# Performance work log

Measured on AMD Instinct MI355X. Metric: run time of the kernel, lower is better.

The kernel has to match this reference:

```python
import jax, jax.numpy as jnp
import numpy as np

N = 2048      # nodes: 8 sequences x 256 tokens
E = 524288    # edges: dense attention graph, 8 * 256^2
H = 8         # heads
DK = 64       # per-head dim


def setup_inputs() -> dict:
    key = jax.random.key(0)
    k1, k2, k3, k4, k5 = jax.random.split(key, 5)
    q = jax.random.normal(k1, (N, H, DK), dtype=jnp.float32)
    k = jax.random.normal(k2, (N, H, DK), dtype=jnp.float32)
    v = jax.random.normal(k3, (N, H, DK), dtype=jnp.float32)
    edge_src = jax.random.randint(k4, (E,), 0, N, dtype=jnp.int32)
    edge_dst = jax.random.randint(k5, (E,), 0, N, dtype=jnp.int32)
    return {"q": q, "k": k, "v": v, "edge_src": edge_src, "edge_dst": edge_dst}


def reference(q, k, v, edge_src, edge_dst):
    # src_dot_dst('k','q','score'): per-edge dot product over head dim -> [E, H]
    score = jnp.einsum('ehd,ehd->eh', k[edge_src], q[edge_dst])
    # scaled_exp('score', sqrt(d_k)): exp(clamp(score / sqrt(d_k), -10, 10))
    score = jnp.exp(jnp.clip(score / jnp.sqrt(jnp.float32(DK)), -10.0, 10.0))
    # send_and_recv: wv = sum_dst(v_src * score), z = sum_dst(score)
    wv = jax.ops.segment_sum(v[edge_src] * score[:, :, None], edge_dst, num_segments=N)  # [N, H, DK]
    z = jax.ops.segment_sum(score, edge_dst, num_segments=N)  # [N, H]
    # post_func normalization: attention output per node
    return wv / z[:, :, None]
```

## Files before the change

kernel.cpp:

```cpp
#include <hip/hip_runtime.h>

#define NNODES 2048
#define NHEAD 8
#define DKDIM 64

typedef unsigned int uint;
typedef unsigned short ushort;
typedef unsigned char uchar;
typedef __fp16 h2 __attribute__((ext_vector_type(2)));
typedef __fp16 h8 __attribute__((ext_vector_type(8)));
typedef float f16v __attribute__((ext_vector_type(16)));

#define KSCALE 0.18033688011112042f
#define CLAMP2 14.426950408889634f

__device__ __forceinline__ uint pk2(float a, float b) {
    union { h2 h; uint u; } x; x.h = __builtin_amdgcn_cvt_pkrtz(a, b); return x.u;
}

__global__ void prep1(const float* __restrict__ k, uint4* __restrict__ kc,
                      uint4* __restrict__ A4) {
    int i = blockIdx.x * 256 + threadIdx.x;
    int dim8 = i & 7, node = (i >> 3) & 2047, h = i >> 14;
    const float* src = k + (size_t)node * 512 + h * 64 + dim8 * 8;
    float4 f0 = *(const float4*)src;
    float4 f1 = *(const float4*)(src + 4);
    uint4 o;
    o.x = pk2(f0.x * KSCALE, f0.y * KSCALE);
    o.y = pk2(f0.z * KSCALE, f0.w * KSCALE);
    o.z = pk2(f1.x * KSCALE, f1.y * KSCALE);
    o.w = pk2(f1.z * KSCALE, f1.w * KSCALE);
    kc[(h * 2048 + node) * 8 + dim8] = o;
    uint4 zz = {0u, 0u, 0u, 0u};
    A4[i] = zz;
}

__global__ void prep2(const float* __restrict__ v, ushort* __restrict__ vt,
                      const int* __restrict__ es, const int* __restrict__ ed,
                      uint* __restrict__ A32, int E) {
    __shared__ float tile[64][65];
    int b = blockIdx.x;
    int t = threadIdx.x;
    if (b < 256) {
        int h = b & 7, tn = b >> 3;
        int nl = t >> 2, dq = (t & 3) * 16;
        const float* src = v + ((size_t)(tn * 64 + nl)) * 512 + h * 64 + dq;
#pragma unroll
        for (int i = 0; i < 4; ++i) {
            float4 f = *(const float4*)(src + i * 4);
            tile[nl][dq + i * 4 + 0] = f.x;
            tile[nl][dq + i * 4 + 1] = f.y;
            tile[nl][dq + i * 4 + 2] = f.z;
            tile[nl][dq + i * 4 + 3] = f.w;
        }
        __syncthreads();
        int dim = t >> 2, nq = (t & 3) * 16;
        uint wv[8];
#pragma unroll
        for (int i = 0; i < 8; ++i)
            wv[i] = pk2(tile[nq + 2 * i][dim], tile[nq + 2 * i + 1][dim]);
        char* base = (char*)vt + ((size_t)(b & 7) * 64 + dim) * 4096 + (b >> 3) * 128;
        int nb0 = (t & 3) * 2;
        uint4 lo = { wv[0], wv[1], wv[2], wv[3] };
        uint4 hi = { wv[4], wv[5], wv[6], wv[7] };
        *(uint4*)(base + nb0 * 16) = lo;
        *(uint4*)(base + nb0 * 16 + 16) = hi;
    } else {
        int i = (b - 256) * 256 + t;
        if (i < E) {
            uint idx = (uint)ed[i] * 2048u + (uint)es[i];
            atomicAdd(&A32[idx >> 3], 1u << ((idx & 7) * 4));
        }
    }
}

__global__ void __launch_bounds__(512, 4) attn_kernel(
    const float* __restrict__ q, const ushort* __restrict__ kc, const ushort* __restrict__ vt,
    const uchar* __restrict__ A8, float* __restrict__ out) {
    __shared__ __align__(16) char LK[2][2][8192];
    __shared__ __align__(16) char LV[2][2][8192];

    int b = blockIdx.x;
    int j = b & 7, idx = b >> 3;
    int dt = (j & 3) * 8 + (idx >> 2);
    int h = (j >> 2) * 4 + (idx & 3);
    int dst0 = dt * 64;
    int t = threadIdx.x;
    int w = t >> 6, half = w >> 2;
    int u = w & 3, sr = u >> 1, dc = u & 1;
    int l = t & 63, lm = l & 31, hi = l >> 5;
    int ht = t & 255;

    const char* kH = (const char*)kc + (size_t)h * 262144;
    const char* vH = (const char*)vt + (size_t)h * 262144;
    const char* aRow = (const char*)A8 + (size_t)(dst0 + dc * 32 + lm) * 1024 + sr * 16;

    h8 qf[4];
    {
        const float* qp = q + (size_t)(dst0 + dc * 32 + lm) * 512 + h * 64 + hi * 8;
#pragma unroll
        for (int jq = 0; jq < 4; ++jq) {
            float4 f0 = *(const float4*)(qp + jq * 16);
            float4 f1 = *(const float4*)(qp + jq * 16 + 4);
            union { uint u4[4]; h8 v; } U;
            U.u4[0] = pk2(f0.x, f0.y); U.u4[1] = pk2(f0.z, f0.w);
            U.u4[2] = pk2(f1.x, f1.y); U.u4[3] = pk2(f1.z, f1.w);
            qf[jq] = U.v;
        }
    }

    f16v of[2];
#pragma unroll
    for (int dg = 0; dg < 2; ++dg)
#pragma unroll
        for (int i = 0; i < 16; ++i) of[dg][i] = 0.f;
    float z = 0.f;

    int r0 = ht >> 3, b0 = ht & 7;
    int ts0 = half * 16;
    uint4 kr[2], vr[2];
    uint4 ac, an;

#pragma unroll
    for (int jj = 0; jj < 2; ++jj) {
        int row = r0 + jj * 32;
        kr[jj] = *(const uint4*)(kH + (size_t)(ts0 * 64 + row) * 128 + b0 * 16);
        vr[jj] = *(const uint4*)(vH + (size_t)row * 4096 + ts0 * 128 + b0 * 16);
        *(uint4*)(LK[half][0] + row * 128 + (b0 ^ (row & 7)) * 16) = kr[jj];
        *(uint4*)(LV[half][0] + row * 128 + (b0 ^ (row & 7)) * 16) = vr[jj];
    }
    ac = *(const uint4*)(aRow + ts0 * 32);
    __syncthreads();

    for (int it = 0; it < 16; ++it) {
        int cur = it & 1;
        int ts = ts0 + it;
        if (it < 15) {
#pragma unroll
            for (int jj = 0; jj < 2; ++jj) {
                int row = r0 + jj * 32;
                kr[jj] = *(const uint4*)(kH + (size_t)((ts + 1) * 64 + row) * 128 + b0 * 16);
                vr[jj] = *(const uint4*)(vH + (size_t)row * 4096 + (ts + 1) * 128 + b0 * 16);
            }
            an = *(const uint4*)(aRow + (ts + 1) * 32);
        }

        f16v sacc;
#pragma unroll
        for (int i = 0; i < 16; ++i) sacc[i] = 0.f;
        __builtin_amdgcn_s_setprio(1);
#pragma unroll
        for (int jq = 0; jq < 4; ++jq) {
            h8 kf = *(const h8*)(LK[half][cur] + (sr * 32 + lm) * 128 +
                                 (((2 * jq + hi) ^ (lm & 7)) * 16));
            sacc = __builtin_amdgcn_mfma_f32_32x32x16_f16(kf, qf[jq], sacc, 0, 0, 0);
        }
        __builtin_amdgcn_s_setprio(0);

        uint W[4][2];
        {
            const uint* aw4 = (const uint*)&ac;
#pragma unroll
            for (int G = 0; G < 4; ++G) {
                uint aw = aw4[G];
                float ee[4];
#pragma unroll
                for (int j2 = 0; j2 < 4; ++j2) {
                    float sc = fminf(fmaxf(sacc[4 * G + j2], -CLAMP2), CLAMP2);
                    ee[j2] = exp2f(sc) * (float)((aw >> (16 * hi + 4 * j2)) & 15u);
                    z += ee[j2];
                }
                W[G][0] = pk2(ee[0], ee[1]);
                W[G][1] = pk2(ee[2], ee[3]);
            }
        }
        uint Wx[4][2];
#pragma unroll
        for (int G = 0; G < 4; ++G) {
            Wx[G][0] = __shfl_xor(W[G][0], 32);
            Wx[G][1] = __shfl_xor(W[G][1], 32);
        }

        __builtin_amdgcn_s_setprio(1);
#pragma unroll
        for (int ks = 0; ks < 2; ++ks) {
            union { uint u4[4]; h8 v; } S;
            S.u4[0] = hi ? Wx[2 * ks + 1][0] : W[2 * ks][0];
            S.u4[1] = hi ? Wx[2 * ks + 1][1] : W[2 * ks][1];
            S.u4[2] = hi ? W[2 * ks + 1][0] : Wx[2 * ks][0];
            S.u4[3] = hi ? W[2 * ks + 1][1] : Wx[2 * ks][1];
#pragma unroll
            for (int dg = 0; dg < 2; ++dg) {
                h8 vf = *(const h8*)(LV[half][cur] + (dg * 32 + lm) * 128 +
                                     (((sr * 4 + ks * 2 + hi) ^ (lm & 7)) * 16));
                of[dg] = __builtin_amdgcn_mfma_f32_32x32x16_f16(vf, S.v, of[dg], 0, 0, 0);
            }
        }
        __builtin_amdgcn_s_setprio(0);

        if (it < 15) {
            int nb = cur ^ 1;
#pragma unroll
            for (int jj = 0; jj < 2; ++jj) {
                int row = r0 + jj * 32;
                *(uint4*)(LK[half][nb] + row * 128 + (b0 ^ (row & 7)) * 16) = kr[jj];
                *(uint4*)(LV[half][nb] + row * 128 + (b0 ^ (row & 7)) * 16) = vr[jj];
            }
            ac = an;
        }
        __syncthreads();
    }

    z += __shfl_xor(z, 32);

    float* CL = (float*)&LK[0][0][0];
    float* CLz = (float*)&LV[0][0][0];
    int gid = half * 2 + sr;
    for (int p = 0; p < 4; ++p) {
        if (gid == p) {
#pragma unroll
            for (int dg = 0; dg < 2; ++dg)
#pragma unroll
                for (int reg = 0; reg < 16; ++reg) {
                    int dim = dg * 32 + (reg & 3) + 8 * (reg >> 2) + 4 * hi;
                    int idx2 = (dc * 32 + lm) * 68 + dim;
                    if (p == 0) CL[idx2] = of[dg][reg];
                    else CL[idx2] += of[dg][reg];
                }
            if (hi == 0) {
                if (p == 0) CLz[dc * 32 + lm] = z;
                else CLz[dc * 32 + lm] += z;
            }
        }
        __syncthreads();
    }

    {
        int dst = t >> 3, d8 = t & 7;
        float inv = 1.0f / CLz[dst];
        float4 o0 = *(float4*)(CL + dst * 68 + d8 * 8);
        float4 o1 = *(float4*)(CL + dst * 68 + d8 * 8 + 4);
        o0.x *= inv; o0.y *= inv; o0.z *= inv; o0.w *= inv;
        o1.x *= inv; o1.y *= inv; o1.z *= inv; o1.w *= inv;
        float* op = out + (size_t)(dst0 + dst) * 512 + h * 64 + d8 * 8;
        *(float4*)op = o0;
        *(float4*)(op + 4) = o1;
    }
}


extern "C" void kernel_launch(void* const* d_in, const int* in_sizes, int n_in,
                              void* d_out, int out_size, void* d_ws, size_t ws_size,
                              hipStream_t stream) {
    const float* q = (const float*)d_in[0];
    const float* k = (const float*)d_in[1];
    const float* v = (const float*)d_in[2];
    const int* esrc = (const int*)d_in[3];
    const int* edst = (const int*)d_in[4];
    float* out = (float*)d_out;
    const int E = in_sizes[3];

    uchar* A8 = (uchar*)d_ws;
    ushort* kc = (ushort*)(A8 + (size_t)NNODES * NNODES / 2);
    ushort* vt = kc + (size_t)NHEAD * NNODES * DKDIM;

    prep1<<<512, 256, 0, stream>>>(k, (uint4*)kc, (uint4*)A8);
    prep2<<<2304, 256, 0, stream>>>(v, vt, esrc, edst, (uint*)A8, E);
    attn_kernel<<<256, 512, 0, stream>>>(q, kc, vt, A8, out);
}
```

Before: 63.64 us.

## Pre-swizzle K/V into MFMA fragment layout and load directly to registers

The prep kernels now write K and V in the exact per-lane MFMA operand order, so the attention kernel loads fragments straight from global memory into registers. This drops the LDS double-buffering and the per-iteration __syncthreads. The K and V prep and the adjacency zeroing are merged into one kernel, and the edge histogram moves to its own launch. Launch bounds are lowered to 2 blocks per SM to make room for more registers. The cost is global-load latency that is only partly hidden by prefetching K one step ahead, while V is loaded in the same iteration it is used.

Measured after the change: 55.49 us. -12.8%, faster.

```diff
diff --git a/kernel.cpp b/kernel.cpp
--- a/kernel.cpp
+++ b/kernel.cpp
@@ -18,33 +18,31 @@
     union { h2 h; uint u; } x; x.h = __builtin_amdgcn_cvt_pkrtz(a, b); return x.u;
 }
 
-__global__ void prep1(const float* __restrict__ k, uint4* __restrict__ kc,
-                      uint4* __restrict__ A4) {
-    int i = blockIdx.x * 256 + threadIdx.x;
-    int dim8 = i & 7, node = (i >> 3) & 2047, h = i >> 14;
-    const float* src = k + (size_t)node * 512 + h * 64 + dim8 * 8;
-    float4 f0 = *(const float4*)src;
-    float4 f1 = *(const float4*)(src + 4);
-    uint4 o;
-    o.x = pk2(f0.x * KSCALE, f0.y * KSCALE);
-    o.y = pk2(f0.z * KSCALE, f0.w * KSCALE);
-    o.z = pk2(f1.x * KSCALE, f1.y * KSCALE);
-    o.w = pk2(f1.z * KSCALE, f1.w * KSCALE);
-    kc[(h * 2048 + node) * 8 + dim8] = o;
-    uint4 zz = {0u, 0u, 0u, 0u};
-    A4[i] = zz;
-}
-
-__global__ void prep2(const float* __restrict__ v, ushort* __restrict__ vt,
-                      const int* __restrict__ es, const int* __restrict__ ed,
-                      uint* __restrict__ A32, int E) {
+__global__ void prep12(const float* __restrict__ k, const float* __restrict__ v,
+                       uint4* __restrict__ kc4, uint4* __restrict__ vt4,
+                       uint4* __restrict__ A4) {
     __shared__ float tile[64][65];
-    int b = blockIdx.x;
-    int t = threadIdx.x;
-    if (b < 256) {
-        int h = b & 7, tn = b >> 3;
+    int b = blockIdx.x, t = threadIdx.x;
+    if (b < 512) {
+        int i = b * 256 + t;
+        int f = i >> 6, l = i & 63;
+        int jq = f & 3, sr = (f >> 2) & 1, ts = (f >> 3) & 31, h = f >> 8;
+        int node = ts * 64 + sr * 32 + (l & 31);
+        int dim0 = (2 * jq + (l >> 5)) * 8;
+        const float* src = k + (size_t)node * 512 + h * 64 + dim0;
+        float4 f0 = *(const float4*)src;
+        float4 f1 = *(const float4*)(src + 4);
+        uint4 o;
+        o.x = pk2(f0.x * KSCALE, f0.y * KSCALE);
+        o.y = pk2(f0.z * KSCALE, f0.w * KSCALE);
+        o.z = pk2(f1.x * KSCALE, f1.y * KSCALE);
+        o.w = pk2(f1.z * KSCALE, f1.w * KSCALE);
+        kc4[(size_t)f * 64 + l] = o;
+    } else if (b < 768) {
+        int bv = b - 512;
+        int h = bv & 7, tn = bv >> 3;
         int nl = t >> 2, dq = (t & 3) * 16;
-        const float* src = v + ((size_t)(tn * 64 + nl)) * 512 + h * 64 + dq;
+        const float* src = v + (size_t)(tn * 64 + nl) * 512 + h * 64 + dq;
 #pragma unroll
         for (int i = 0; i < 4; ++i) {
             float4 f = *(const float4*)(src + i * 4);
@@ -54,31 +52,42 @@
             tile[nl][dq + i * 4 + 3] = f.w;
         }
         __syncthreads();
-        int dim = t >> 2, nq = (t & 3) * 16;
-        uint wv[8];
-#pragma unroll
-        for (int i = 0; i < 8; ++i)
-            wv[i] = pk2(tile[nq + 2 * i][dim], tile[nq + 2 * i + 1][dim]);
-        char* base = (char*)vt + ((size_t)(b & 7) * 64 + dim) * 4096 + (b >> 3) * 128;
-        int nb0 = (t & 3) * 2;
-        uint4 lo = { wv[0], wv[1], wv[2], wv[3] };
-        uint4 hi = { wv[4], wv[5], wv[6], wv[7] };
-        *(uint4*)(base + nb0 * 16) = lo;
-        *(uint4*)(base + nb0 * 16 + 16) = hi;
+#pragma unroll
+        for (int rep = 0; rep < 2; ++rep) {
+            int slot = rep * 256 + t;
+            int fsub = slot >> 6, l = slot & 63;
+            int srv = fsub >> 2, ks = (fsub >> 1) & 1, dg = fsub & 1;
+            int dim = dg * 32 + (l & 31);
+            int s8 = (srv * 4 + ks * 2 + (l >> 5)) * 8;
+            uint4 o;
+            o.x = pk2(tile[s8 + 0][dim], tile[s8 + 1][dim]);
+            o.y = pk2(tile[s8 + 2][dim], tile[s8 + 3][dim]);
+            o.z = pk2(tile[s8 + 4][dim], tile[s8 + 5][dim]);
+            o.w = pk2(tile[s8 + 6][dim], tile[s8 + 7][dim]);
+            int fV = (h * 32 + tn) * 8 + srv * 4 + ks * 2 + dg;
+            vt4[(size_t)fV * 64 + l] = o;
+        }
     } else {
-        int i = (b - 256) * 256 + t;
-        if (i < E) {
-            uint idx = (uint)ed[i] * 2048u + (uint)es[i];
-            atomicAdd(&A32[idx >> 3], 1u << ((idx & 7) * 4));
-        }
-    }
-}
-
-__global__ void __launch_bounds__(512, 4) attn_kernel(
-    const float* __restrict__ q, const ushort* __restrict__ kc, const ushort* __restrict__ vt,
+        uint4 zz = {0u, 0u, 0u, 0u};
+        A4[(size_t)(b - 768) * 512 + t] = zz;
+        A4[(size_t)(b - 768) * 512 + t + 256] = zz;
+    }
+}
+
+__global__ void histA(const int* __restrict__ es, const int* __restrict__ ed,
+                      uint* __restrict__ A32, int E) {
+    int i = blockIdx.x * 256 + threadIdx.x;
+    if (i < E) {
+        uint idx = (uint)ed[i] * 2048u + (uint)es[i];
+        atomicAdd(&A32[idx >> 3], 1u << ((idx & 7) * 4));
+    }
+}
+
+__global__ void __launch_bounds__(512, 2) attn_kernel(
+    const float* __restrict__ q, const char* __restrict__ kc, const char* __restrict__ vt,
     const uchar* __restrict__ A8, float* __restrict__ out) {
-    __shared__ __align__(16) char LK[2][2][8192];
-    __shared__ __align__(16) char LV[2][2][8192];
+    __shared__ float CL[64 * 68];
+    __shared__ float CLz[64];
 
     int b = blockIdx.x;
     int j = b & 7, idx = b >> 3;
@@ -89,11 +98,12 @@
     int w = t >> 6, half = w >> 2;
     int u = w & 3, sr = u >> 1, dc = u & 1;
     int l = t & 63, lm = l & 31, hi = l >> 5;
-    int ht = t & 255;
-
-    const char* kH = (const char*)kc + (size_t)h * 262144;
-    const char* vH = (const char*)vt + (size_t)h * 262144;
-    const char* aRow = (const char*)A8 + (size_t)(dst0 + dc * 32 + lm) * 1024 + sr * 16;
+
+    int ts0 = half * 16;
+    const char* kBase = kc + ((size_t)(h * 32 + ts0) * 8 + sr * 4) * 1024 + l * 16;
+    const char* vBase = vt + ((size_t)(h * 32 + ts0) * 8 + sr * 4) * 1024 + l * 16;
+    const char* aRow = (const char*)A8 + (size_t)(dst0 + dc * 32 + lm) * 1024 + sr * 16
+                       + ts0 * 32;
 
     h8 qf[4];
     {
@@ -116,34 +126,23 @@
         for (int i = 0; i < 16; ++i) of[dg][i] = 0.f;
     float z = 0.f;
 
-    int r0 = ht >> 3, b0 = ht & 7;
-    int ts0 = half * 16;
-    uint4 kr[2], vr[2];
+    uint4 kcur[4], knxt[4], vcur[4];
     uint4 ac, an;
 
 #pragma unroll
-    for (int jj = 0; jj < 2; ++jj) {
-        int row = r0 + jj * 32;
-        kr[jj] = *(const uint4*)(kH + (size_t)(ts0 * 64 + row) * 128 + b0 * 16);
-        vr[jj] = *(const uint4*)(vH + (size_t)row * 4096 + ts0 * 128 + b0 * 16);
-        *(uint4*)(LK[half][0] + row * 128 + (b0 ^ (row & 7)) * 16) = kr[jj];
-        *(uint4*)(LV[half][0] + row * 128 + (b0 ^ (row & 7)) * 16) = vr[jj];
-    }
-    ac = *(const uint4*)(aRow + ts0 * 32);
-    __syncthreads();
+    for (int jq = 0; jq < 4; ++jq)
+        kcur[jq] = *(const uint4*)(kBase + jq * 1024);
+    ac = *(const uint4*)aRow;
 
     for (int it = 0; it < 16; ++it) {
-        int cur = it & 1;
-        int ts = ts0 + it;
-        if (it < 15) {
-#pragma unroll
-            for (int jj = 0; jj < 2; ++jj) {
-                int row = r0 + jj * 32;
-                kr[jj] = *(const uint4*)(kH + (size_t)((ts + 1) * 64 + row) * 128 + b0 * 16);
-                vr[jj] = *(const uint4*)(vH + (size_t)row * 4096 + (ts + 1) * 128 + b0 * 16);
-            }
-            an = *(const uint4*)(aRow + (ts + 1) * 32);
-        }
+        size_t toff = (size_t)it * 8192;
+#pragma unroll
+        for (int ks = 0; ks < 2; ++ks)
+#pragma unroll
+            for (int dg = 0; dg < 2; ++dg)
+                vcur[ks * 2 + dg] = *(const uint4*)(vBase + toff + (ks * 2 + dg) * 1024);
+        int itn = (it < 15) ? it + 1 : it;
+        an = *(const uint4*)(aRow + itn * 32);
 
         f16v sacc;
 #pragma unroll
@@ -151,11 +150,14 @@
         __builtin_amdgcn_s_setprio(1);
 #pragma unroll
         for (int jq = 0; jq < 4; ++jq) {
-            h8 kf = *(const h8*)(LK[half][cur] + (sr * 32 + lm) * 128 +
-                                 (((2 * jq + hi) ^ (lm & 7)) * 16));
-            sacc = __builtin_amdgcn_mfma_f32_32x32x16_f16(kf, qf[jq], sacc, 0, 0, 0);
+            union { uint4 u; h8 v; } KF; KF.u = kcur[jq];
+            sacc = __builtin_amdgcn_mfma_f32_32x32x16_f16(KF.v, qf[jq], sacc, 0, 0, 0);
         }
         __builtin_amdgcn_s_setprio(0);
+
+#pragma unroll
+        for (int jq = 0; jq < 4; ++jq)
+            knxt[jq] = *(const uint4*)(kBase + (size_t)itn * 8192 + jq * 1024);
 
         uint W[4][2];
         {
@@ -191,30 +193,19 @@
             S.u4[3] = hi ? W[2 * ks + 1][1] : Wx[2 * ks][1];
 #pragma unroll
             for (int dg = 0; dg < 2; ++dg) {
-                h8 vf = *(const h8*)(LV[half][cur] + (dg * 32 + lm) * 128 +
-                                     (((sr * 4 + ks * 2 + hi) ^ (lm & 7)) * 16));
-                of[dg] = __builtin_amdgcn_mfma_f32_32x32x16_f16(vf, S.v, of[dg], 0, 0, 0);
+                union { uint4 u; h8 v; } VF; VF.u = vcur[ks * 2 + dg];
+                of[dg] = __builtin_amdgcn_mfma_f32_32x32x16_f16(VF.v, S.v, of[dg], 0, 0, 0);
             }
         }
         __builtin_amdgcn_s_setprio(0);
 
-        if (it < 15) {
-            int nb = cur ^ 1;
-#pragma unroll
-            for (int jj = 0; jj < 2; ++jj) {
-                int row = r0 + jj * 32;
-                *(uint4*)(LK[half][nb] + row * 128 + (b0 ^ (row & 7)) * 16) = kr[jj];
-                *(uint4*)(LV[half][nb] + row * 128 + (b0 ^ (row & 7)) * 16) = vr[jj];
-            }
-            ac = an;
-        }
-        __syncthreads();
+#pragma unroll
+        for (int jq = 0; jq < 4; ++jq) kcur[jq] = knxt[jq];
+        ac = an;
     }
 
     z += __shfl_xor(z, 32);
 
-    float* CL = (float*)&LK[0][0][0];
-    float* CLz = (float*)&LV[0][0][0];
     int gid = half * 2 + sr;
     for (int p = 0; p < 4; ++p) {
         if (gid == p) {
@@ -261,10 +252,10 @@
     const int E = in_sizes[3];
 
     uchar* A8 = (uchar*)d_ws;
-    ushort* kc = (ushort*)(A8 + (size_t)NNODES * NNODES / 2);
-    ushort* vt = kc + (size_t)NHEAD * NNODES * DKDIM;
-
-    prep1<<<512, 256, 0, stream>>>(k, (uint4*)kc, (uint4*)A8);
-    prep2<<<2304, 256, 0, stream>>>(v, vt, esrc, edst, (uint*)A8, E);
+    char* kc = (char*)(A8 + (size_t)NNODES * NNODES / 2);
+    char* vt = kc + (size_t)NHEAD * NNODES * DKDIM * 2;
+
+    prep12<<<1024, 256, 0, stream>>>(k, v, (uint4*)kc, (uint4*)vt, (uint4*)A8);
+    histA<<<(E + 255) / 256, 256, 0, stream>>>(esrc, edst, (uint*)A8, E);
     attn_kernel<<<256, 512, 0, stream>>>(q, kc, vt, A8, out);
 }
```
